# Optimization experiments

Hardware: AMD Instinct MI355X
Metric: run time of the kernel (lower is better)

The kernel has to match this reference:

```python
import jax, jax.numpy as jnp
import numpy as np

NUM_TIMES = 1024  # times are drawn from [0, 1024), used as fixed segment count
N = 16777216


def setup_inputs() -> dict:
    key = jax.random.key(0)
    k1, k2, k3 = jax.random.split(key, 3)
    outs = jax.random.normal(k1, (N,), dtype=jnp.float32)
    T_E = jax.random.randint(k2, (N,), 0, 2, dtype=jnp.int32)
    T_T = jax.random.randint(k3, (N,), 0, NUM_TIMES, dtype=jnp.int32)
    return {"outs": outs, "T_E": T_E, "T_T": T_T}


def reference(outs, T_E, T_T):
    # E[E > 0] = 1  -> binary event indicator
    E = (T_E > 0).astype(outs.dtype)
    # Y_label_T = |T_T| ; integer times act directly as segment ids
    seg_ids = jnp.abs(T_T)
    Obs = jnp.sum(E)
    # log of running sum of hazards: log(cumsum(exp(yhat)))
    y_hat_cumsum = jnp.log(jnp.cumsum(jnp.exp(outs)))
    # original segment_max initializes accumulator at 0, so it is clipped below at 0;
    # jnp.maximum also neutralizes -inf fill for empty segments (count=0 there anyway)
    seg_max = jnp.maximum(
        jax.ops.segment_max(y_hat_cumsum, seg_ids, num_segments=NUM_TIMES), 0.0
    )
    seg_cnt = jax.ops.segment_sum(E, seg_ids, num_segments=NUM_TIMES)
    loss_s2 = jnp.sum(seg_max * seg_cnt)
    loss_s1 = jnp.sum(outs * E)
    return (loss_s2 - loss_s1) / Obs
```

## Files before the change

kernel.cpp:

```cpp
#include <hip/hip_runtime.h>

#define NUM_SEGS 1024
#define CHUNK_LOG 13
#define CHUNK (1 << CHUNK_LOG)
#define SUBCH 4
#define SUPER (CHUNK * SUBCH)
#define BLK 256

__device__ __forceinline__ float waveReduceSumF(float v) {
#pragma unroll
    for (int off = 32; off > 0; off >>= 1) v += __shfl_down(v, off, 64);
    return v;
}
__device__ __forceinline__ unsigned waveReduceSumU(unsigned v) {
#pragma unroll
    for (int off = 32; off > 0; off >>= 1) v += __shfl_down(v, off, 64);
    return v;
}

__global__ void init_kernel(unsigned* __restrict__ seg_cnt,
                            int* __restrict__ last_idx,
                            unsigned* __restrict__ obs,
                            double* __restrict__ loss1,
                            double* __restrict__ loss2) {
    int t = blockIdx.x * blockDim.x + threadIdx.x;
    if (t < NUM_SEGS) { seg_cnt[t] = 0u; last_idx[t] = -1; }
    if (t == 0) { obs[0] = 0u; loss1[0] = 0.0; loss2[0] = 0.0; }
}

__global__ __launch_bounds__(BLK) void pass1_kernel(
    const float* __restrict__ outs, const int* __restrict__ te,
    const int* __restrict__ tt, int N, int nChunks,
    float* __restrict__ chunk_sums, unsigned* __restrict__ seg_cnt,
    int* __restrict__ last_idx, unsigned* __restrict__ obs,
    double* __restrict__ loss1) {
    __shared__ unsigned hist[NUM_SEGS];
    __shared__ int lmax[NUM_SEGS];
    __shared__ float redF[BLK / 64];
    __shared__ unsigned redU[BLK / 64];

    for (int t = threadIdx.x; t < NUM_SEGS; t += BLK) { hist[t] = 0u; lmax[t] = -1; }
    __syncthreads();

    float sumOE = 0.f;
    unsigned cntE = 0u;
    const int superBase = blockIdx.x * SUPER;
    const int lane = threadIdx.x & 63;
    const int wid = threadIdx.x >> 6;

#pragma unroll 1
    for (int k = 0; k < SUBCH; ++k) {
        const int cbase = superBase + k * CHUNK;
        float sumExp = 0.f;
        if (cbase + CHUNK <= N) {
#pragma unroll
            for (int it = 0; it < CHUNK / (BLK * 4); ++it) {
                const int i = cbase + it * (BLK * 4) + (threadIdx.x << 2);
                const float4 o = *reinterpret_cast<const float4*>(outs + i);
                const int4 ev = *reinterpret_cast<const int4*>(te + i);
                const int4 sv = *reinterpret_cast<const int4*>(tt + i);
                const float e0 = __expf(o.x), e1 = __expf(o.y);
                const float e2 = __expf(o.z), e3 = __expf(o.w);
                sumExp += (e0 + e1) + (e2 + e3);
                const int s0 = sv.x < 0 ? -sv.x : sv.x;
                const int s1 = sv.y < 0 ? -sv.y : sv.y;
                const int s2 = sv.z < 0 ? -sv.z : sv.z;
                const int s3 = sv.w < 0 ? -sv.w : sv.w;
                atomicMax(&lmax[s0], i);
                atomicMax(&lmax[s1], i + 1);
                atomicMax(&lmax[s2], i + 2);
                atomicMax(&lmax[s3], i + 3);
                if (ev.x > 0) { cntE++; sumOE += o.x; atomicAdd(&hist[s0], 1u); }
                if (ev.y > 0) { cntE++; sumOE += o.y; atomicAdd(&hist[s1], 1u); }
                if (ev.z > 0) { cntE++; sumOE += o.z; atomicAdd(&hist[s2], 1u); }
                if (ev.w > 0) { cntE++; sumOE += o.w; atomicAdd(&hist[s3], 1u); }
            }
        } else {
            const int end = (cbase + CHUNK < N) ? cbase + CHUNK : N;
            for (int i = cbase + (int)threadIdx.x; i < end; i += BLK) {
                const float o = outs[i];
                const int e = te[i];
                int s = tt[i]; s = s < 0 ? -s : s;
                sumExp += __expf(o);
                atomicMax(&lmax[s], i);
                if (e > 0) { cntE++; sumOE += o; atomicAdd(&hist[s], 1u); }
            }
        }
        const float w = waveReduceSumF(sumExp);
        if (lane == 0) redF[wid] = w;
        __syncthreads();
        if (threadIdx.x == 0) {
            const float s4 = (redF[0] + redF[1]) + (redF[2] + redF[3]);
            const int cidx = cbase >> CHUNK_LOG;
            if (cidx < nChunks) chunk_sums[cidx] = s4;
        }
        __syncthreads();
    }

    for (int t = threadIdx.x; t < NUM_SEGS; t += BLK) {
        const unsigned h = hist[t];
        if (h) atomicAdd(&seg_cnt[t], h);
        const int m = lmax[t];
        if (m >= 0) atomicMax(&last_idx[t], m);
    }

    const float wOE = waveReduceSumF(sumOE);
    const unsigned wC = waveReduceSumU(cntE);
    if (lane == 0) { redF[wid] = wOE; redU[wid] = wC; }
    __syncthreads();
    if (threadIdx.x == 0) {
        const float oe = (redF[0] + redF[1]) + (redF[2] + redF[3]);
        const unsigned c = redU[0] + redU[1] + redU[2] + redU[3];
        atomicAdd(loss1, (double)oe);
        atomicAdd(obs, c);
    }
}

__global__ void scan_kernel(const float* __restrict__ csums,
                            double* __restrict__ cprefix, int nChunks) {
    __shared__ double tsum[256];
    const int per = (nChunks + 255) / 256;
    const int start = threadIdx.x * per;
    double s = 0.0;
    for (int j = 0; j < per; ++j) {
        const int c = start + j;
        if (c < nChunks) s += (double)csums[c];
    }
    tsum[threadIdx.x] = s;
    __syncthreads();
    if (threadIdx.x == 0) {
        double acc = 0.0;
        for (int i = 0; i < 256; ++i) { const double t = tsum[i]; tsum[i] = acc; acc += t; }
    }
    __syncthreads();
    double acc = tsum[threadIdx.x];
    for (int j = 0; j < per; ++j) {
        const int c = start + j;
        if (c < nChunks) { cprefix[c] = acc; acc += (double)csums[c]; }
    }
}

__global__ __launch_bounds__(256) void seg_kernel(
    const float* __restrict__ outs, const int* __restrict__ last_idx,
    const unsigned* __restrict__ seg_cnt, const double* __restrict__ cprefix,
    double* __restrict__ loss2) {
    __shared__ float redF[4];
    const int t = blockIdx.x;
    const int li = last_idx[t];
    if (li < 0) return;
    const int c = li >> CHUNK_LOG;
    const int base = c << CHUNK_LOG;
    float s = 0.f;
    for (int i = base + (int)threadIdx.x; i <= li; i += 256) s += __expf(outs[i]);
    const float w = waveReduceSumF(s);
    const int lane = threadIdx.x & 63, wid = threadIdx.x >> 6;
    if (lane == 0) redF[wid] = w;
    __syncthreads();
    if (threadIdx.x == 0) {
        const double S = cprefix[c] + (double)((redF[0] + redF[1]) + (redF[2] + redF[3]));
        double sm = log(S);
        if (sm < 0.0) sm = 0.0;
        atomicAdd(loss2, sm * (double)seg_cnt[t]);
    }
}

__global__ void final_kernel(const double* __restrict__ loss1,
                             const double* __restrict__ loss2,
                             const unsigned* __restrict__ obs,
                             float* __restrict__ out) {
    out[0] = (float)((loss2[0] - loss1[0]) / (double)obs[0]);
}

extern "C" void kernel_launch(void* const* d_in, const int* in_sizes, int n_in,
                              void* d_out, int out_size, void* d_ws, size_t ws_size,
                              hipStream_t stream) {
    const float* outs = (const float*)d_in[0];
    const int* te = (const int*)d_in[1];
    const int* tt = (const int*)d_in[2];
    const int N = in_sizes[0];
    float* out = (float*)d_out;

    const int nChunks = (N + CHUNK - 1) / CHUNK;

    char* ws = (char*)d_ws;
    double* d_loss1 = (double*)ws;
    double* d_loss2 = d_loss1 + 1;
    double* d_cprefix = (double*)(ws + 16);
    float* d_csums = (float*)(d_cprefix + nChunks);
    int* d_lastidx = (int*)(d_csums + nChunks);
    unsigned* d_segcnt = (unsigned*)(d_lastidx + NUM_SEGS);
    unsigned* d_obs = d_segcnt + NUM_SEGS;

    init_kernel<<<(NUM_SEGS + 255) / 256, 256, 0, stream>>>(d_segcnt, d_lastidx,
                                                            d_obs, d_loss1, d_loss2);
    const int nSuper = (N + SUPER - 1) / SUPER;
    pass1_kernel<<<nSuper, BLK, 0, stream>>>(outs, te, tt, N, nChunks, d_csums,
                                             d_segcnt, d_lastidx, d_obs, d_loss1);
    scan_kernel<<<1, 256, 0, stream>>>(d_csums, d_cprefix, nChunks);
    seg_kernel<<<NUM_SEGS, 256, 0, stream>>>(outs, d_lastidx, d_segcnt, d_cprefix,
                                             d_loss2);
    final_kernel<<<1, 1, 0, stream>>>(d_loss1, d_loss2, d_obs, out);
}
```

Baseline: 234.2 us.

## Track last chunk via byte flags, fuse scan, segment and final kernels

Replaces the per-segment shared-memory atomicMax of the element index with plain byte stores recording the latest subchunk, so pass1 only learns the last chunk per segment. A fused segment kernel then sums the preceding chunk totals in double per segment, rescans that chunk to find the exact last index, and computes the partial exp sum. The final result is written by the last block through a done counter. Pass1 also grows to 1024-thread blocks. The aim is to cut shared-atomic contention in the hot pass and save two kernel launches, at the cost of redundant prefix sums and chunk rescans in each of the 1024 segment blocks.

```diff
diff --git a/kernel.cpp b/kernel.cpp
--- a/kernel.cpp
+++ b/kernel.cpp
@@ -5,41 +5,59 @@
 #define CHUNK (1 << CHUNK_LOG)
 #define SUBCH 4
 #define SUPER (CHUNK * SUBCH)
-#define BLK 256
+#define BLK 1024
+#define NWAVE (BLK / 64)
+#define SEGBLK 256
 
 __device__ __forceinline__ float waveReduceSumF(float v) {
 #pragma unroll
     for (int off = 32; off > 0; off >>= 1) v += __shfl_down(v, off, 64);
     return v;
 }
+__device__ __forceinline__ double waveReduceSumD(double v) {
+#pragma unroll
+    for (int off = 32; off > 0; off >>= 1) v += __shfl_down(v, off, 64);
+    return v;
+}
 __device__ __forceinline__ unsigned waveReduceSumU(unsigned v) {
 #pragma unroll
     for (int off = 32; off > 0; off >>= 1) v += __shfl_down(v, off, 64);
     return v;
 }
+__device__ __forceinline__ int waveReduceMaxI(int v) {
+#pragma unroll
+    for (int off = 32; off > 0; off >>= 1) {
+        const int o = __shfl_down(v, off, 64);
+        v = o > v ? o : v;
+    }
+    return v;
+}
 
 __global__ void init_kernel(unsigned* __restrict__ seg_cnt,
-                            int* __restrict__ last_idx,
+                            int* __restrict__ last_chunk,
                             unsigned* __restrict__ obs,
                             double* __restrict__ loss1,
-                            double* __restrict__ loss2) {
-    int t = blockIdx.x * blockDim.x + threadIdx.x;
-    if (t < NUM_SEGS) { seg_cnt[t] = 0u; last_idx[t] = -1; }
-    if (t == 0) { obs[0] = 0u; loss1[0] = 0.0; loss2[0] = 0.0; }
-}
-
-__global__ __launch_bounds__(BLK) void pass1_kernel(
+                            double* __restrict__ loss2,
+                            unsigned* __restrict__ done) {
+    const int t = blockIdx.x * blockDim.x + threadIdx.x;
+    if (t < NUM_SEGS) { seg_cnt[t] = 0u; last_chunk[t] = -1; }
+    if (t == 0) { obs[0] = 0u; loss1[0] = 0.0; loss2[0] = 0.0; done[0] = 0u; }
+}
+
+__global__ __launch_bounds__(BLK, 8) void pass1_kernel(
     const float* __restrict__ outs, const int* __restrict__ te,
     const int* __restrict__ tt, int N, int nChunks,
     float* __restrict__ chunk_sums, unsigned* __restrict__ seg_cnt,
-    int* __restrict__ last_idx, unsigned* __restrict__ obs,
+    int* __restrict__ last_chunk, unsigned* __restrict__ obs,
     double* __restrict__ loss1) {
     __shared__ unsigned hist[NUM_SEGS];
-    __shared__ int lmax[NUM_SEGS];
-    __shared__ float redF[BLK / 64];
-    __shared__ unsigned redU[BLK / 64];
-
-    for (int t = threadIdx.x; t < NUM_SEGS; t += BLK) { hist[t] = 0u; lmax[t] = -1; }
+    __shared__ unsigned char flags[NUM_SEGS];
+    __shared__ float redF[NWAVE];
+    __shared__ unsigned redU[NWAVE];
+
+    for (int t = threadIdx.x; t < NUM_SEGS; t += BLK) hist[t] = 0u;
+    if (threadIdx.x < NUM_SEGS / 4)
+        reinterpret_cast<unsigned*>(flags)[threadIdx.x] = 0xFFFFFFFFu;
     __syncthreads();
 
     float sumOE = 0.f;
@@ -66,10 +84,10 @@
                 const int s1 = sv.y < 0 ? -sv.y : sv.y;
                 const int s2 = sv.z < 0 ? -sv.z : sv.z;
                 const int s3 = sv.w < 0 ? -sv.w : sv.w;
-                atomicMax(&lmax[s0], i);
-                atomicMax(&lmax[s1], i + 1);
-                atomicMax(&lmax[s2], i + 2);
-                atomicMax(&lmax[s3], i + 3);
+                flags[s0] = (unsigned char)k;
+                flags[s1] = (unsigned char)k;
+                flags[s2] = (unsigned char)k;
+                flags[s3] = (unsigned char)k;
                 if (ev.x > 0) { cntE++; sumOE += o.x; atomicAdd(&hist[s0], 1u); }
                 if (ev.y > 0) { cntE++; sumOE += o.y; atomicAdd(&hist[s1], 1u); }
                 if (ev.z > 0) { cntE++; sumOE += o.z; atomicAdd(&hist[s2], 1u); }
@@ -82,7 +100,7 @@
                 const int e = te[i];
                 int s = tt[i]; s = s < 0 ? -s : s;
                 sumExp += __expf(o);
-                atomicMax(&lmax[s], i);
+                flags[s] = (unsigned char)k;
                 if (e > 0) { cntE++; sumOE += o; atomicAdd(&hist[s], 1u); }
             }
         }
@@ -90,18 +108,21 @@
         if (lane == 0) redF[wid] = w;
         __syncthreads();
         if (threadIdx.x == 0) {
-            const float s4 = (redF[0] + redF[1]) + (redF[2] + redF[3]);
+            float s4 = 0.f;
+#pragma unroll
+            for (int j = 0; j < NWAVE; ++j) s4 += redF[j];
             const int cidx = cbase >> CHUNK_LOG;
             if (cidx < nChunks) chunk_sums[cidx] = s4;
         }
         __syncthreads();
     }
 
+    const int chunk0 = blockIdx.x * SUBCH;
     for (int t = threadIdx.x; t < NUM_SEGS; t += BLK) {
         const unsigned h = hist[t];
         if (h) atomicAdd(&seg_cnt[t], h);
-        const int m = lmax[t];
-        if (m >= 0) atomicMax(&last_idx[t], m);
+        const unsigned f = flags[t];
+        if (f != 0xFFu) atomicMax(&last_chunk[t], chunk0 + (int)f);
     }
 
     const float wOE = waveReduceSumF(sumOE);
@@ -109,66 +130,81 @@
     if (lane == 0) { redF[wid] = wOE; redU[wid] = wC; }
     __syncthreads();
     if (threadIdx.x == 0) {
-        const float oe = (redF[0] + redF[1]) + (redF[2] + redF[3]);
-        const unsigned c = redU[0] + redU[1] + redU[2] + redU[3];
+        float oe = 0.f; unsigned c = 0u;
+#pragma unroll
+        for (int j = 0; j < NWAVE; ++j) { oe += redF[j]; c += redU[j]; }
         atomicAdd(loss1, (double)oe);
         atomicAdd(obs, c);
     }
 }
 
-__global__ void scan_kernel(const float* __restrict__ csums,
-                            double* __restrict__ cprefix, int nChunks) {
-    __shared__ double tsum[256];
-    const int per = (nChunks + 255) / 256;
-    const int start = threadIdx.x * per;
-    double s = 0.0;
-    for (int j = 0; j < per; ++j) {
-        const int c = start + j;
-        if (c < nChunks) s += (double)csums[c];
-    }
-    tsum[threadIdx.x] = s;
-    __syncthreads();
+__global__ __launch_bounds__(SEGBLK) void seg_final_kernel(
+    const float* __restrict__ outs, const int* __restrict__ tt,
+    const float* __restrict__ csums, const unsigned* __restrict__ seg_cnt,
+    const int* __restrict__ last_chunk, const double* __restrict__ loss1,
+    double* __restrict__ loss2, const unsigned* __restrict__ obs,
+    unsigned* __restrict__ done, float* __restrict__ out, int N) {
+    __shared__ double redD[SEGBLK / 64];
+    __shared__ float redF[SEGBLK / 64];
+    __shared__ int redI[SEGBLK / 64];
+    __shared__ int s_li;
+
+    const int t = blockIdx.x;
+    const unsigned cnt = seg_cnt[t];
+    const int lane = threadIdx.x & 63, wid = threadIdx.x >> 6;
+
+    if (cnt != 0u) {
+        const int lc = last_chunk[t];
+        double p = 0.0;
+        for (int c = threadIdx.x; c < lc; c += SEGBLK) p += (double)csums[c];
+        p = waveReduceSumD(p);
+        if (lane == 0) redD[wid] = p;
+
+        const int base = lc << CHUNK_LOG;
+        const int end = (base + CHUNK < N) ? base + CHUNK : N;
+        int li = -1;
+        for (int i = base + (int)threadIdx.x; i < end; i += SEGBLK) {
+            int s = tt[i]; s = s < 0 ? -s : s;
+            if (s == t) li = i;
+        }
+        li = waveReduceMaxI(li);
+        if (lane == 0) redI[wid] = li;
+        __syncthreads();
+        if (threadIdx.x == 0) {
+            int m = redI[0];
+#pragma unroll
+            for (int j = 1; j < SEGBLK / 64; ++j) m = redI[j] > m ? redI[j] : m;
+            s_li = m;
+        }
+        __syncthreads();
+        const int LI = s_li;
+
+        float fs = 0.f;
+        for (int i = base + (int)threadIdx.x; i <= LI; i += SEGBLK) fs += __expf(outs[i]);
+        fs = waveReduceSumF(fs);
+        if (lane == 0) redF[wid] = fs;
+        __syncthreads();
+        if (threadIdx.x == 0 && LI >= 0) {
+            double pre = 0.0;
+            float fsum = 0.f;
+#pragma unroll
+            for (int j = 0; j < SEGBLK / 64; ++j) { pre += redD[j]; fsum += redF[j]; }
+            double sm = log(pre + (double)fsum);
+            if (sm < 0.0) sm = 0.0;
+            atomicAdd(loss2, sm * (double)cnt);
+        }
+    }
+
     if (threadIdx.x == 0) {
-        double acc = 0.0;
-        for (int i = 0; i < 256; ++i) { const double t = tsum[i]; tsum[i] = acc; acc += t; }
-    }
-    __syncthreads();
-    double acc = tsum[threadIdx.x];
-    for (int j = 0; j < per; ++j) {
-        const int c = start + j;
-        if (c < nChunks) { cprefix[c] = acc; acc += (double)csums[c]; }
-    }
-}
-
-__global__ __launch_bounds__(256) void seg_kernel(
-    const float* __restrict__ outs, const int* __restrict__ last_idx,
-    const unsigned* __restrict__ seg_cnt, const double* __restrict__ cprefix,
-    double* __restrict__ loss2) {
-    __shared__ float redF[4];
-    const int t = blockIdx.x;
-    const int li = last_idx[t];
-    if (li < 0) return;
-    const int c = li >> CHUNK_LOG;
-    const int base = c << CHUNK_LOG;
-    float s = 0.f;
-    for (int i = base + (int)threadIdx.x; i <= li; i += 256) s += __expf(outs[i]);
-    const float w = waveReduceSumF(s);
-    const int lane = threadIdx.x & 63, wid = threadIdx.x >> 6;
-    if (lane == 0) redF[wid] = w;
-    __syncthreads();
-    if (threadIdx.x == 0) {
-        const double S = cprefix[c] + (double)((redF[0] + redF[1]) + (redF[2] + redF[3]));
-        double sm = log(S);
-        if (sm < 0.0) sm = 0.0;
-        atomicAdd(loss2, sm * (double)seg_cnt[t]);
-    }
-}
-
-__global__ void final_kernel(const double* __restrict__ loss1,
-                             const double* __restrict__ loss2,
-                             const unsigned* __restrict__ obs,
-                             float* __restrict__ out) {
-    out[0] = (float)((loss2[0] - loss1[0]) / (double)obs[0]);
+        __threadfence();
+        const unsigned d = atomicAdd(done, 1u);
+        if (d == (unsigned)(gridDim.x - 1)) {
+            const double l2 = atomicAdd(loss2, 0.0);
+            const double l1 = loss1[0];
+            const unsigned o = obs[0];
+            out[0] = (float)((l2 - l1) / (double)o);
+        }
+    }
 }
 
 extern "C" void kernel_launch(void* const* d_in, const int* in_sizes, int n_in,
@@ -185,19 +221,18 @@
     char* ws = (char*)d_ws;
     double* d_loss1 = (double*)ws;
     double* d_loss2 = d_loss1 + 1;
-    double* d_cprefix = (double*)(ws + 16);
-    float* d_csums = (float*)(d_cprefix + nChunks);
-    int* d_lastidx = (int*)(d_csums + nChunks);
-    unsigned* d_segcnt = (unsigned*)(d_lastidx + NUM_SEGS);
-    unsigned* d_obs = d_segcnt + NUM_SEGS;
-
-    init_kernel<<<(NUM_SEGS + 255) / 256, 256, 0, stream>>>(d_segcnt, d_lastidx,
-                                                            d_obs, d_loss1, d_loss2);
+    float* d_csums = (float*)(ws + 16);
+    unsigned* d_segcnt = (unsigned*)(d_csums + nChunks);
+    int* d_lastchunk = (int*)(d_segcnt + NUM_SEGS);
+    unsigned* d_obs = (unsigned*)(d_lastchunk + NUM_SEGS);
+    unsigned* d_done = d_obs + 1;
+
+    init_kernel<<<(NUM_SEGS + 255) / 256, 256, 0, stream>>>(
+        d_segcnt, d_lastchunk, d_obs, d_loss1, d_loss2, d_done);
     const int nSuper = (N + SUPER - 1) / SUPER;
     pass1_kernel<<<nSuper, BLK, 0, stream>>>(outs, te, tt, N, nChunks, d_csums,
-                                             d_segcnt, d_lastidx, d_obs, d_loss1);
-    scan_kernel<<<1, 256, 0, stream>>>(d_csums, d_cprefix, nChunks);
-    seg_kernel<<<NUM_SEGS, 256, 0, stream>>>(outs, d_lastidx, d_segcnt, d_cprefix,
-                                             d_loss2);
-    final_kernel<<<1, 1, 0, stream>>>(d_loss1, d_loss2, d_obs, out);
-}
+                                             d_segcnt, d_lastchunk, d_obs, d_loss1);
+    seg_final_kernel<<<NUM_SEGS, SEGBLK, 0, stream>>>(
+        outs, tt, d_csums, d_segcnt, d_lastchunk, d_loss1, d_loss2, d_obs, d_done,
+        out, N);
+}
```

Result: slower. 240.0 us (+2.5%).
